# Optimization experiments

Measured on AMD Instinct MI355X. Metric: run time of the kernel, lower is better.

## Reference

```python
import jax, jax.numpy as jnp
import numpy as np

DIM = 512
HEADS = 8
B, H, W = 8, 32, 32
SMOOTH = 1e-4
BN_EPS = 1e-5


def _conv(x, w, pad):
    return jax.lax.conv_general_dilated(
        x, w, window_strides=(1, 1), padding=[(pad, pad), (pad, pad)],
        dimension_numbers=('NCHW', 'OIHW', 'NCHW'))


def setup_inputs() -> dict:
    key = jax.random.key(0)
    k1, k2, k3 = jax.random.split(key, 3)
    x = jax.random.normal(k1, (B, DIM, H, W), dtype=jnp.float32)
    # conv weights with fan-in style scaling for stable magnitudes
    W_qkv = jax.random.normal(k2, (3 * DIM, DIM, 3, 3), dtype=jnp.float32) * (1.0 / np.sqrt(DIM * 9))
    W_out = jax.random.normal(k3, (DIM, DIM, 1, 1), dtype=jnp.float32) * (1.0 / np.sqrt(DIM))
    gamma = jnp.ones((DIM,), dtype=jnp.float32)
    beta = jnp.zeros((DIM,), dtype=jnp.float32)
    return {"x": x, "W_qkv": W_qkv, "W_out": W_out, "gamma": gamma, "beta": beta}


def reference(x, W_qkv, W_out, gamma, beta):
    b, c, h, w = x.shape
    g = HEADS
    d = c // g
    n = h * w
    qkv = _conv(x, W_qkv, pad=1)                      # [b, 3c, h, w]
    q, k, v = jnp.split(qkv, 3, axis=1)
    # 'b (g d) h w -> b g (h w) d'
    to_seq = lambda t: t.reshape(b, g, d, n).transpose(0, 1, 3, 2)
    q, k, v = to_seq(q), to_seq(k), to_seq(v)         # [b, g, n, d]
    attn = jnp.einsum('bgid,bgjd->bgij', q, k)        # [b, g, n, n]
    qn = jnp.sqrt(jnp.sum(q * q, axis=-1) + SMOOTH)   # [b, g, n]
    kn = jnp.sqrt(jnp.sum(k * k, axis=-1) + SMOOTH)   # [b, g, n]
    attn = attn / (qn[:, :, :, None] * kn[:, :, None, :] + SMOOTH)
    out = jnp.einsum('bgij,bgjd->bgid', attn, v)      # [b, g, n, d]
    # 'b g (h w) d -> b (g d) h w'
    out = out.transpose(0, 1, 3, 2).reshape(b, c, h, w)
    out = _conv(out, W_out, pad=0)
    # BatchNorm2d (training mode: batch statistics, biased variance)
    mean = jnp.mean(out, axis=(0, 2, 3))
    var = jnp.var(out, axis=(0, 2, 3))
    out = (out - mean[None, :, None, None]) * jax.lax.rsqrt(var + BN_EPS)[None, :, None, None]
    out = out * gamma[None, :, None, None] + beta[None, :, None, None]
    return jax.nn.relu(out)
```

## Files before the change

kernel.cpp:

```cpp
#include <hip/hip_runtime.h>
#include <math.h>


#define SMOOTH 1e-4f
#define BN_EPS 1e-5f

typedef __attribute__((ext_vector_type(8))) short bf16x8;
typedef __attribute__((ext_vector_type(8))) unsigned short u16x8;
typedef __attribute__((ext_vector_type(4))) float f32x4;
typedef __attribute__((ext_vector_type(4))) unsigned int u32x4;
typedef __attribute__((ext_vector_type(4))) unsigned short u16x4;

__device__ inline unsigned short bf16rne(float f) {
  unsigned int u = __float_as_uint(f);
  u += 0x7fff + ((u >> 16) & 1);
  return (unsigned short)(u >> 16);
}
__device__ inline float b2f(unsigned short u) {
  return __uint_as_float((unsigned int)u << 16);
}

typedef __attribute__((address_space(1))) void gvoid;
typedef __attribute__((address_space(3))) void lvoid;
__device__ __forceinline__ void async16(const void* g, void* l) {
  __builtin_amdgcn_global_load_lds((gvoid*)g, (lvoid*)l, 16, 0, 0);
}

__global__ void prep_kernel(const float* __restrict__ wq,
                            unsigned short* __restrict__ wqr2,
                            const float* __restrict__ x,
                            unsigned short* __restrict__ xrp2,
                            const float* __restrict__ wo,
                            unsigned short* __restrict__ wor,
                            float* __restrict__ sums,
                            float* __restrict__ sumsq) {
  __shared__ float Sh[32 * 292];
  const int tid = threadIdx.x;
  const int bid = blockIdx.x;
  if (bid < 768) {
    const int cotile = bid / 32;
    const int rem = bid - cotile * 32;
    const int ci0c = rem >> 1, cohalf = rem & 1;
#pragma unroll
    for (int k = 0; k < 9; ++k) {
      int idx = tid + k * 256;
      int row = idx / 72, col = idx - row * 72;
      *(float4*)(Sh + row * 292 + col * 4) =
          *(const float4*)(wq +
                           (size_t)(cotile * 64 + cohalf * 32 + row) * 4608 +
                           ci0c * 288 + col * 4);
    }
    __syncthreads();
    const size_t wbase = (size_t)(ci0c * 24 + cotile) * 18432;
#pragma unroll
    for (int k = 0; k < 5; ++k) {
      int j = tid + k * 256;
      if (j < 1152) {
        int co_l = j & 31;
        int g36 = j >> 5;
        int c4 = g36 / 9, tt = g36 - c4 * 9;
        u16x8 pk;
#pragma unroll
        for (int e = 0; e < 8; ++e)
          pk[e] = bf16rne(Sh[co_l * 292 + (c4 * 8 + e) * 9 + tt]);
        *(u16x8*)(wqr2 + wbase +
                  (size_t)((c4 * 9 + tt) * 64 + cohalf * 32 + co_l) * 8) = pk;
      }
    }
  } else if (bid < 1280) {
    const int bx = bid - 768;
    const int p0 = (bx & 7) * 128;
    const int ci0 = ((bx >> 3) & 7) * 64;
    const int b = bx >> 6;
    for (int k = 0; k < 8; ++k) {
      int idx = tid + k * 256;
      int c4 = idx & 31, row = idx >> 5;
      *(float4*)(Sh + row * 132 + c4 * 4) =
          *(const float4*)(x + ((size_t)(b * 512 + ci0 + row)) * 1024 + p0 + c4 * 4);
    }
    __syncthreads();
    const int pl = tid >> 1, half = tid & 1;
    const int p = p0 + pl;
    const int h = p >> 5, w = p & 31;
#pragma unroll
    for (int v = 0; v < 8; ++v) {
      u16x4 pk;
#pragma unroll
      for (int e = 0; e < 4; ++e)
        pk[e] = bf16rne(Sh[(half * 32 + v * 4 + e) * 132 + pl]);
      int cc = ci0 + half * 32 + v * 4;
      int ci0c = cc >> 5, c4 = (cc >> 3) & 3, e0 = cc & 7;
      size_t gran =
          (size_t)((ci0c * 4 + c4) * 8 + b) * 1156 + (h + 1) * 34 + (w + 1);
      *(u16x4*)(xrp2 + gran * 8 + e0) = pk;
    }
  } else {
    const int rb = bid - 1280;
    int idx = rb * 256 + tid;
    wor[idx] = bf16rne(wo[idx]);
    if (rb < 2) {
      sums[idx] = 0.f;
      sumsq[idx] = 0.f;
    }
  }
}

__global__ __launch_bounds__(256) void conv3x3_mfma(
    const unsigned short* __restrict__ wqr2,
    const unsigned short* __restrict__ xrp2,
    unsigned short* __restrict__ qt, unsigned short* __restrict__ kt,
    unsigned short* __restrict__ vt, float* __restrict__ rqn,
    float* __restrict__ rkn) {
  __shared__ __align__(16) unsigned short Wl[2304 * 8];
  __shared__ __align__(16) unsigned short Xl[4 * 256 * 8];
  __shared__ float Snl[128];

  const int tid = threadIdx.x;
  const int lane = tid & 63;
  const int wave = tid >> 6;
  const int wco = (wave & 1) * 32;
  const int wn = (wave >> 1) * 64;
  const int l15 = lane & 15;
  const int quad = lane >> 4;
  const int h0 = blockIdx.x * 4;
  const int co0 = blockIdx.y * 64;
  const int b = blockIdx.z;

  f32x4 acc[2][4];
  for (int ma = 0; ma < 2; ++ma)
    for (int nb = 0; nb < 4; ++nb) acc[ma][nb] = (f32x4){0.f, 0.f, 0.f, 0.f};

  for (int ci0 = 0; ci0 < 512; ci0 += 32) {
    const int ci0c = ci0 >> 5;
    __syncthreads();
    const unsigned short* wsrc =
        wqr2 + (size_t)(ci0c * 24 + (co0 >> 6)) * 18432;
    {
      int cbase = wave * 9;
#pragma unroll
      for (int j = 0; j < 9; ++j) {
        int c = cbase + j;
        async16(wsrc + (size_t)c * 512 + lane * 8, Wl + (size_t)c * 512);
      }
    }
    const unsigned short* xsrc =
        xrp2 + ((size_t)((ci0c * 4 + wave) * 8 + b) * 1156 + h0 * 34) * 8;
#pragma unroll
    for (int j = 0; j < 4; ++j)
      async16(xsrc + (size_t)j * 512 + lane * 8,
              Xl + (size_t)(wave * 256 + j * 64) * 8);
    __syncthreads();

#pragma unroll
    for (int t = 0; t < 9; ++t) {
      const int ky = t / 3, kx = t - ky * 3;
      bf16x8 af[2], bfr[4];
#pragma unroll
      for (int ma = 0; ma < 2; ++ma)
        af[ma] = *(const bf16x8*)(
            Wl + (size_t)((quad * 9 + t) * 64 + wco + ma * 16 + l15) * 8);
#pragma unroll
      for (int nb = 0; nb < 4; ++nb) {
        int n = wn + nb * 16 + l15;
        int hh = (n >> 5) + ky;
        int wi = (n & 31) + kx;
        bfr[nb] = *(const bf16x8*)(Xl + (size_t)(quad * 256 + hh * 34 + wi) * 8);
      }
#pragma unroll
      for (int ma = 0; ma < 2; ++ma)
#pragma unroll
        for (int nb = 0; nb < 4; ++nb)
          acc[ma][nb] = __builtin_amdgcn_mfma_f32_16x16x32_bf16(
              af[ma], bfr[nb], acc[ma][nb], 0, 0, 0);
    }
  }

  const int sec = co0 >> 9;
  const int g = (co0 & 511) >> 6;
  const int bg = b * 8 + g;
  if (sec < 2) {
    unsigned short* dst = (sec == 0) ? qt : kt;
#pragma unroll
    for (int ma = 0; ma < 2; ++ma)
#pragma unroll
      for (int nb = 0; nb < 4; ++nb) {
        int n = wn + nb * 16 + l15;
        int p = (h0 + (n >> 5)) * 32 + (n & 31);
        int db = wco + ma * 16 + quad * 4;
        u16x4 pk;
#pragma unroll
        for (int r = 0; r < 4; ++r) pk[r] = bf16rne(acc[ma][nb][r]);
        *(u16x4*)(dst + ((size_t)bg * 1024 + p) * 64 + db) = pk;
      }
    float ps[4];
#pragma unroll
    for (int nb = 0; nb < 4; ++nb) {
      float s = 0.f;
#pragma unroll
      for (int ma = 0; ma < 2; ++ma)
#pragma unroll
        for (int r = 0; r < 4; ++r) s = fmaf(acc[ma][nb][r], acc[ma][nb][r], s);
      s += __shfl_down(s, 32);
      s += __shfl_down(s, 16);
      ps[nb] = s;
    }
    if (wco == 0 && quad == 0)
#pragma unroll
      for (int nb = 0; nb < 4; ++nb) Snl[wn + nb * 16 + l15] = ps[nb];
    __syncthreads();
    if (wco == 32 && quad == 0) {
      float* ndst = (sec == 0) ? rqn : rkn;
#pragma unroll
      for (int nb = 0; nb < 4; ++nb) {
        int n = wn + nb * 16 + l15;
        int p = (h0 + (n >> 5)) * 32 + (n & 31);
        ndst[bg * 1024 + p] = rsqrtf(Snl[n] + ps[nb] + SMOOTH);
      }
    }
  } else {
#pragma unroll
    for (int ma = 0; ma < 2; ++ma)
#pragma unroll
      for (int nb = 0; nb < 4; ++nb) {
        int n = wn + nb * 16 + l15;
        int p = (h0 + (n >> 5)) * 32 + (n & 31);
#pragma unroll
        for (int r = 0; r < 4; ++r) {
          int d = wco + ma * 16 + quad * 4 + r;
          vt[((size_t)bg * 64 + d) * 1024 + p] = bf16rne(acc[ma][nb][r]);
        }
      }
  }
}

__global__ __launch_bounds__(128) void attn_mfma(
    const unsigned short* __restrict__ qt, const unsigned short* __restrict__ kt,
    const unsigned short* __restrict__ vt, const float* __restrict__ rqn,
    const float* __restrict__ rkn, unsigned short* __restrict__ aob) {
  __shared__ __align__(16) unsigned short Kl[64 * 72];
  __shared__ __align__(16) unsigned short Vl[64 * 72];
  __shared__ __align__(16) unsigned short Sl[64 * 72];

  const int tid = threadIdx.x;
  const int lane = tid & 63, wave = tid >> 6;
  const int l15 = lane & 15, quad = lane >> 4;
  const int bg = blockIdx.x;
  const int i0 = blockIdx.y * 64;
  const int iw = i0 + wave * 32;
  const int b = bg >> 3, g = bg & 7;

  int srow[4], sperm[4], sc8[4];
#pragma unroll
  for (int s = 0; s < 4; ++s) {
    int gidx = tid + s * 128;
    sc8[s] = gidx & 7;
    srow[s] = gidx >> 3;
    sperm[s] = (srow[s] & 3) * 16 + (srow[s] >> 2);
  }

  bf16x8 qf[2][2];
#pragma unroll
  for (int ma = 0; ma < 2; ++ma)
#pragma unroll
    for (int ks = 0; ks < 2; ++ks)
      qf[ma][ks] = *(const bf16x8*)(
          qt + ((size_t)bg * 1024 + iw + ma * 16 + l15) * 64 + ks * 32 + quad * 8);

  float rq[2][4];
#pragma unroll
  for (int ma = 0; ma < 2; ++ma)
#pragma unroll
    for (int r = 0; r < 4; ++r)
      rq[ma][r] = rqn[bg * 1024 + iw + ma * 16 + quad * 4 + r];

  f32x4 oacc[2][4];
  for (int mf = 0; mf < 2; ++mf)
    for (int nf = 0; nf < 4; ++nf) oacc[mf][nf] = (f32x4){0.f, 0.f, 0.f, 0.f};

  unsigned short* Sw = Sl + wave * 32 * 72;

  u32x4 rk[4], rv[4];
#pragma unroll
  for (int s = 0; s < 4; ++s) {
    rk[s] = *(const u32x4*)(kt + ((size_t)bg * 1024 + srow[s]) * 64 + sc8[s] * 8);
    rv[s] = *(const u32x4*)(vt + ((size_t)bg * 64 + srow[s]) * 1024 + sc8[s] * 8);
  }

  for (int jt = 0; jt < 16; ++jt) {
    const int j0 = jt * 64;
    __syncthreads();
#pragma unroll
    for (int s = 0; s < 4; ++s) {
      *(u32x4*)(Kl + sperm[s] * 72 + sc8[s] * 8) = rk[s];
      *(u32x4*)(Vl + srow[s] * 72 + sc8[s] * 8) = rv[s];
    }
    u32x4 nk[4], nv[4];
    if (jt < 15) {
      const int j1 = j0 + 64;
#pragma unroll
      for (int s = 0; s < 4; ++s) {
        nk[s] = *(const u32x4*)(kt + ((size_t)bg * 1024 + j1 + srow[s]) * 64 + sc8[s] * 8);
        nv[s] = *(const u32x4*)(vt + ((size_t)bg * 64 + srow[s]) * 1024 + j1 + sc8[s] * 8);
      }
    }
    __syncthreads();

    f32x4 sacc[2][4];
    for (int ma = 0; ma < 2; ++ma)
      for (int nb = 0; nb < 4; ++nb) sacc[ma][nb] = (f32x4){0.f, 0.f, 0.f, 0.f};
#pragma unroll
    for (int ks = 0; ks < 2; ++ks) {
#pragma unroll
      for (int nb = 0; nb < 4; ++nb) {
        bf16x8 kf = *(const bf16x8*)(Kl + (nb * 16 + l15) * 72 + ks * 32 + quad * 8);
#pragma unroll
        for (int ma = 0; ma < 2; ++ma)
          sacc[ma][nb] = __builtin_amdgcn_mfma_f32_16x16x32_bf16(
              qf[ma][ks], kf, sacc[ma][nb], 0, 0, 0);
      }
    }

    float4 rk4 = *(const float4*)(rkn + bg * 1024 + j0 + 4 * l15);
#pragma unroll
    for (int ma = 0; ma < 2; ++ma)
#pragma unroll
      for (int r = 0; r < 4; ++r) {
        u16x4 pk;
        pk[0] = bf16rne(sacc[ma][0][r] * (rq[ma][r] * rk4.x));
        pk[1] = bf16rne(sacc[ma][1][r] * (rq[ma][r] * rk4.y));
        pk[2] = bf16rne(sacc[ma][2][r] * (rq[ma][r] * rk4.z));
        pk[3] = bf16rne(sacc[ma][3][r] * (rq[ma][r] * rk4.w));
        *(u16x4*)(Sw + (ma * 16 + quad * 4 + r) * 72 + 4 * l15) = pk;
      }
#pragma unroll
    for (int ks2 = 0; ks2 < 2; ++ks2) {
      bf16x8 sa[2];
#pragma unroll
      for (int mf = 0; mf < 2; ++mf)
        sa[mf] = *(const bf16x8*)(Sw + (mf * 16 + l15) * 72 + ks2 * 32 + quad * 8);
#pragma unroll
      for (int nf = 0; nf < 4; ++nf) {
        bf16x8 vb = *(const bf16x8*)(Vl + (l15 + 16 * nf) * 72 + ks2 * 32 + quad * 8);
#pragma unroll
        for (int mf = 0; mf < 2; ++mf)
          oacc[mf][nf] = __builtin_amdgcn_mfma_f32_16x16x32_bf16(
              sa[mf], vb, oacc[mf][nf], 0, 0, 0);
      }
    }
    if (jt < 15) {
#pragma unroll
      for (int s = 0; s < 4; ++s) {
        rk[s] = nk[s];
        rv[s] = nv[s];
      }
    }
  }

#pragma unroll
  for (int mf = 0; mf < 2; ++mf)
#pragma unroll
    for (int nf = 0; nf < 4; ++nf)
#pragma unroll
      for (int r = 0; r < 4; ++r) {
        int i = iw + mf * 16 + quad * 4 + r;
        int d = l15 + 16 * nf;
        aob[((size_t)(b * 1024) + i) * 512 + g * 64 + d] = bf16rne(oacc[mf][nf][r]);
      }
}

__global__ __launch_bounds__(256) void conv1x1_mfma(
    const unsigned short* __restrict__ wor, const unsigned short* __restrict__ aob,
    unsigned short* __restrict__ yb, float* __restrict__ sums,
    float* __restrict__ sumsq) {
  __shared__ __align__(16) unsigned short Wl[64 * 40];
  __shared__ __align__(16) unsigned short Bl[64 * 40];

  const int tid = threadIdx.x;
  const int lane = tid & 63, wave = tid >> 6;
  const int l15 = lane & 15, quad = lane >> 4;
  const int wco = (wave & 1) * 32;
  const int wp = (wave >> 1) * 32;
  const int p0 = blockIdx.x * 64;
  const int co0 = blockIdx.y * 64;
  const int b = blockIdx.z;

  f32x4 acc[2][2];
  for (int ma = 0; ma < 2; ++ma)
    for (int nb = 0; nb < 2; ++nb) acc[ma][nb] = (f32x4){0.f, 0.f, 0.f, 0.f};

  for (int ci0 = 0; ci0 < 512; ci0 += 32) {
    __syncthreads();
    {
      int c4 = tid & 3, co = tid >> 2;
      *(u32x4*)(Wl + co * 40 + c4 * 8) =
          *(const u32x4*)(wor + (size_t)(co0 + co) * 512 + ci0 + c4 * 8);
      *(u32x4*)(Bl + co * 40 + c4 * 8) =
          *(const u32x4*)(aob + ((size_t)(b * 1024) + p0 + co) * 512 + ci0 + c4 * 8);
    }
    __syncthreads();

    bf16x8 af[2], bf[2];
#pragma unroll
    for (int ma = 0; ma < 2; ++ma)
      af[ma] = *(const bf16x8*)(Wl + (wco + ma * 16 + l15) * 40 + quad * 8);
#pragma unroll
    for (int nb = 0; nb < 2; ++nb)
      bf[nb] = *(const bf16x8*)(Bl + (wp + nb * 16 + l15) * 40 + quad * 8);
#pragma unroll
    for (int ma = 0; ma < 2; ++ma)
#pragma unroll
      for (int nb = 0; nb < 2; ++nb)
        acc[ma][nb] = __builtin_amdgcn_mfma_f32_16x16x32_bf16(
            af[ma], bf[nb], acc[ma][nb], 0, 0, 0);
  }

#pragma unroll
  for (int ma = 0; ma < 2; ++ma)
#pragma unroll
    for (int r = 0; r < 4; ++r) {
      int co = co0 + wco + ma * 16 + quad * 4 + r;
      float s1 = 0.f, s2 = 0.f;
#pragma unroll
      for (int nb = 0; nb < 2; ++nb) {
        float v = acc[ma][nb][r];
        yb[((size_t)(b * 512) + co) * 1024 + p0 + wp + nb * 16 + l15] = bf16rne(v);
        s1 += v;
        s2 = fmaf(v, v, s2);
      }
      for (int off = 8; off >= 1; off >>= 1) {
        s1 += __shfl_down(s1, off, 16);
        s2 += __shfl_down(s2, off, 16);
      }
      if (l15 == 0) {
        atomicAdd(&sums[co], s1);
        atomicAdd(&sumsq[co], s2);
      }
    }
}

__global__ void bn_kernel(const unsigned short* __restrict__ yb,
                          const float* __restrict__ sums,
                          const float* __restrict__ sumsq,
                          const float* __restrict__ gamma,
                          const float* __restrict__ beta,
                          float* __restrict__ out) {
  int idx = blockIdx.x * 256 + threadIdx.x;
  int c = (idx >> 8) & 511;
  u16x4 vb = *(const u16x4*)(yb + (size_t)idx * 4);
  float mean = sums[c] * (1.f / 8192.f);
  float var = sumsq[c] * (1.f / 8192.f) - mean * mean;
  float sc = gamma[c] * rsqrtf(var + BN_EPS);
  float sh = beta[c] - mean * sc;
  float4 r;
  r.x = fmaxf(0.f, fmaf(b2f(vb[0]), sc, sh));
  r.y = fmaxf(0.f, fmaf(b2f(vb[1]), sc, sh));
  r.z = fmaxf(0.f, fmaf(b2f(vb[2]), sc, sh));
  r.w = fmaxf(0.f, fmaf(b2f(vb[3]), sc, sh));
  ((float4*)out)[idx] = r;
}

extern "C" void kernel_launch(void* const* d_in, const int* in_sizes, int n_in,
                              void* d_out, int out_size, void* d_ws,
                              size_t ws_size, hipStream_t stream) {
  const float* x = (const float*)d_in[0];
  const float* wq = (const float*)d_in[1];
  const float* wo = (const float*)d_in[2];
  const float* gamma = (const float*)d_in[3];
  const float* beta = (const float*)d_in[4];
  float* out = (float*)d_out;

  unsigned short* qt = (unsigned short*)d_ws;
  unsigned short* kt = qt + (size_t)4194304;
  unsigned short* vt = kt + (size_t)4194304;
  unsigned short* aob = vt + (size_t)4194304;
  unsigned short* wqr2 = aob + (size_t)4194304;
  unsigned short* wor = wqr2 + (size_t)7077888;
  unsigned short* xrp2 = wor + (size_t)262144;
  float* rqn = (float*)(xrp2 + (size_t)4736000);
  float* rkn = rqn + 65536;
  unsigned short* yb = (unsigned short*)(rkn + 65536);
  float* sums = (float*)(yb + (size_t)4194304);
  float* sumsq = sums + 512;

  hipMemsetAsync(xrp2, 0, (size_t)4736000 * 2, stream);
  prep_kernel<<<dim3(2304), 256, 0, stream>>>(wq, wqr2, x, xrp2, wo, wor, sums,
                                              sumsq);
  conv3x3_mfma<<<dim3(8, 24, 8), 256, 0, stream>>>(wqr2, xrp2, qt, kt, vt, rqn,
                                                   rkn);
  attn_mfma<<<dim3(64, 16), 128, 0, stream>>>(qt, kt, vt, rqn, rkn, aob);
  conv1x1_mfma<<<dim3(16, 8, 8), 256, 0, stream>>>(wor, aob, yb, sums, sumsq);
  bn_kernel<<<dim3(4096), 256, 0, stream>>>(yb, sums, sumsq, gamma, beta, out);
}
```

Measured before the change: 271.6 us.

## Run attention with one wave per block and reuse the K LDS tile for scores

Reworks the attention kernel so each 64-thread block runs a single wave that owns all 64 query rows, instead of two waves splitting them. The K tile buffer also holds the score matrix, and the block-wide barriers plus the register prefetch of the next K/V tile are removed. Because everything runs in one wave, no barriers are needed, and each K/V tile load now feeds twice as many MFMAs. In exchange there are half as many waves in flight, more accumulator registers per wave, and global loads are no longer overlapped with compute through the prefetch.

```diff
diff --git a/kernel.cpp b/kernel.cpp
--- a/kernel.cpp
+++ b/kernel.cpp
@@ -233,88 +233,63 @@
   }
 }
 
-__global__ __launch_bounds__(128) void attn_mfma(
+__global__ __launch_bounds__(64) void attn_mfma(
     const unsigned short* __restrict__ qt, const unsigned short* __restrict__ kt,
     const unsigned short* __restrict__ vt, const float* __restrict__ rqn,
     const float* __restrict__ rkn, unsigned short* __restrict__ aob) {
-  __shared__ __align__(16) unsigned short Kl[64 * 72];
+  __shared__ __align__(16) unsigned short KSl[64 * 74];
   __shared__ __align__(16) unsigned short Vl[64 * 72];
-  __shared__ __align__(16) unsigned short Sl[64 * 72];
-
-  const int tid = threadIdx.x;
-  const int lane = tid & 63, wave = tid >> 6;
+
+  const int lane = threadIdx.x;
   const int l15 = lane & 15, quad = lane >> 4;
   const int bg = blockIdx.x;
   const int i0 = blockIdx.y * 64;
-  const int iw = i0 + wave * 32;
   const int b = bg >> 3, g = bg & 7;
 
-  int srow[4], sperm[4], sc8[4];
-#pragma unroll
-  for (int s = 0; s < 4; ++s) {
-    int gidx = tid + s * 128;
-    sc8[s] = gidx & 7;
-    srow[s] = gidx >> 3;
-    sperm[s] = (srow[s] & 3) * 16 + (srow[s] >> 2);
-  }
-
-  bf16x8 qf[2][2];
-#pragma unroll
-  for (int ma = 0; ma < 2; ++ma)
+  const int c8 = lane & 7;
+  const int r0 = lane >> 3;
+
+  bf16x8 qf[4][2];
+#pragma unroll
+  for (int ma = 0; ma < 4; ++ma)
 #pragma unroll
     for (int ks = 0; ks < 2; ++ks)
       qf[ma][ks] = *(const bf16x8*)(
-          qt + ((size_t)bg * 1024 + iw + ma * 16 + l15) * 64 + ks * 32 + quad * 8);
-
-  float rq[2][4];
-#pragma unroll
-  for (int ma = 0; ma < 2; ++ma)
+          qt + ((size_t)bg * 1024 + i0 + ma * 16 + l15) * 64 + ks * 32 + quad * 8);
+
+  float rq[4][4];
+#pragma unroll
+  for (int ma = 0; ma < 4; ++ma)
 #pragma unroll
     for (int r = 0; r < 4; ++r)
-      rq[ma][r] = rqn[bg * 1024 + iw + ma * 16 + quad * 4 + r];
-
-  f32x4 oacc[2][4];
-  for (int mf = 0; mf < 2; ++mf)
+      rq[ma][r] = rqn[bg * 1024 + i0 + ma * 16 + quad * 4 + r];
+
+  f32x4 oacc[4][4];
+  for (int mf = 0; mf < 4; ++mf)
     for (int nf = 0; nf < 4; ++nf) oacc[mf][nf] = (f32x4){0.f, 0.f, 0.f, 0.f};
-
-  unsigned short* Sw = Sl + wave * 32 * 72;
-
-  u32x4 rk[4], rv[4];
-#pragma unroll
-  for (int s = 0; s < 4; ++s) {
-    rk[s] = *(const u32x4*)(kt + ((size_t)bg * 1024 + srow[s]) * 64 + sc8[s] * 8);
-    rv[s] = *(const u32x4*)(vt + ((size_t)bg * 64 + srow[s]) * 1024 + sc8[s] * 8);
-  }
 
   for (int jt = 0; jt < 16; ++jt) {
     const int j0 = jt * 64;
-    __syncthreads();
-#pragma unroll
-    for (int s = 0; s < 4; ++s) {
-      *(u32x4*)(Kl + sperm[s] * 72 + sc8[s] * 8) = rk[s];
-      *(u32x4*)(Vl + srow[s] * 72 + sc8[s] * 8) = rv[s];
-    }
-    u32x4 nk[4], nv[4];
-    if (jt < 15) {
-      const int j1 = j0 + 64;
-#pragma unroll
-      for (int s = 0; s < 4; ++s) {
-        nk[s] = *(const u32x4*)(kt + ((size_t)bg * 1024 + j1 + srow[s]) * 64 + sc8[s] * 8);
-        nv[s] = *(const u32x4*)(vt + ((size_t)bg * 64 + srow[s]) * 1024 + j1 + sc8[s] * 8);
-      }
-    }
-    __syncthreads();
-
-    f32x4 sacc[2][4];
-    for (int ma = 0; ma < 2; ++ma)
+#pragma unroll
+    for (int s = 0; s < 8; ++s) {
+      int row = r0 + 8 * s;
+      int pr = (row & 3) * 16 + (row >> 2);
+      u32x4 kv = *(const u32x4*)(kt + ((size_t)bg * 1024 + j0 + row) * 64 + c8 * 8);
+      u32x4 vv = *(const u32x4*)(vt + ((size_t)bg * 64 + row) * 1024 + j0 + c8 * 8);
+      *(u32x4*)(KSl + pr * 74 + c8 * 8) = kv;
+      *(u32x4*)(Vl + row * 72 + c8 * 8) = vv;
+    }
+
+    f32x4 sacc[4][4];
+    for (int ma = 0; ma < 4; ++ma)
       for (int nb = 0; nb < 4; ++nb) sacc[ma][nb] = (f32x4){0.f, 0.f, 0.f, 0.f};
 #pragma unroll
     for (int ks = 0; ks < 2; ++ks) {
 #pragma unroll
       for (int nb = 0; nb < 4; ++nb) {
-        bf16x8 kf = *(const bf16x8*)(Kl + (nb * 16 + l15) * 72 + ks * 32 + quad * 8);
-#pragma unroll
-        for (int ma = 0; ma < 2; ++ma)
+        bf16x8 kf = *(const bf16x8*)(KSl + (nb * 16 + l15) * 74 + ks * 32 + quad * 8);
+#pragma unroll
+        for (int ma = 0; ma < 4; ++ma)
           sacc[ma][nb] = __builtin_amdgcn_mfma_f32_16x16x32_bf16(
               qf[ma][ks], kf, sacc[ma][nb], 0, 0, 0);
       }
@@ -322,7 +297,7 @@
 
     float4 rk4 = *(const float4*)(rkn + bg * 1024 + j0 + 4 * l15);
 #pragma unroll
-    for (int ma = 0; ma < 2; ++ma)
+    for (int ma = 0; ma < 4; ++ma)
 #pragma unroll
       for (int r = 0; r < 4; ++r) {
         u16x4 pk;
@@ -330,39 +305,33 @@
         pk[1] = bf16rne(sacc[ma][1][r] * (rq[ma][r] * rk4.y));
         pk[2] = bf16rne(sacc[ma][2][r] * (rq[ma][r] * rk4.z));
         pk[3] = bf16rne(sacc[ma][3][r] * (rq[ma][r] * rk4.w));
-        *(u16x4*)(Sw + (ma * 16 + quad * 4 + r) * 72 + 4 * l15) = pk;
-      }
+        *(u16x4*)(KSl + (ma * 16 + quad * 4 + r) * 74 + 4 * l15) = pk;
+      }
+
 #pragma unroll
     for (int ks2 = 0; ks2 < 2; ++ks2) {
-      bf16x8 sa[2];
-#pragma unroll
-      for (int mf = 0; mf < 2; ++mf)
-        sa[mf] = *(const bf16x8*)(Sw + (mf * 16 + l15) * 72 + ks2 * 32 + quad * 8);
+      bf16x8 sa[4];
+#pragma unroll
+      for (int mf = 0; mf < 4; ++mf)
+        sa[mf] = *(const bf16x8*)(KSl + (mf * 16 + l15) * 74 + ks2 * 32 + quad * 8);
 #pragma unroll
       for (int nf = 0; nf < 4; ++nf) {
         bf16x8 vb = *(const bf16x8*)(Vl + (l15 + 16 * nf) * 72 + ks2 * 32 + quad * 8);
 #pragma unroll
-        for (int mf = 0; mf < 2; ++mf)
+        for (int mf = 0; mf < 4; ++mf)
           oacc[mf][nf] = __builtin_amdgcn_mfma_f32_16x16x32_bf16(
               sa[mf], vb, oacc[mf][nf], 0, 0, 0);
       }
     }
-    if (jt < 15) {
-#pragma unroll
-      for (int s = 0; s < 4; ++s) {
-        rk[s] = nk[s];
-        rv[s] = nv[s];
-      }
-    }
   }
 
 #pragma unroll
-  for (int mf = 0; mf < 2; ++mf)
+  for (int mf = 0; mf < 4; ++mf)
 #pragma unroll
     for (int nf = 0; nf < 4; ++nf)
 #pragma unroll
       for (int r = 0; r < 4; ++r) {
-        int i = iw + mf * 16 + quad * 4 + r;
+        int i = i0 + mf * 16 + quad * 4 + r;
         int d = l15 + 16 * nf;
         aob[((size_t)(b * 1024) + i) * 512 + g * 64 + d] = bf16rne(oacc[mf][nf][r]);
       }
@@ -487,7 +456,7 @@
                                               sumsq);
   conv3x3_mfma<<<dim3(8, 24, 8), 256, 0, stream>>>(wqr2, xrp2, qt, kt, vt, rqn,
                                                    rkn);
-  attn_mfma<<<dim3(64, 16), 128, 0, stream>>>(qt, kt, vt, rqn, rkn, aob);
+  attn_mfma<<<dim3(64, 16), 64, 0, stream>>>(qt, kt, vt, rqn, rkn, aob);
   conv1x1_mfma<<<dim3(16, 8, 8), 256, 0, stream>>>(wor, aob, yb, sums, sumsq);
   bn_kernel<<<dim3(4096), 256, 0, stream>>>(yb, sums, sumsq, gamma, beta, out);
 }
```

After: 314.9 us. 15.9% more time.
